# Performance work log

Hardware: AMD Instinct MI355X
Metric: run time of the kernel (lower is better)

The kernel has to match this reference:

```python
import jax, jax.numpy as jnp
import numpy as np

H = 4096        # hidden_size
I = 11008       # intermediate_size
R = 32          # low-rank error-correction rank
NLEV = 16       # int4 -> 16 levels
Q_ZERO = 7.5    # symmetric int4 zero point
Q_STEP = 0.005  # per-channel scale multiplier (keeps dequantized weights ~N(0, 1/sqrt(H)) scale)
LR_SCALE = 0.02 # low-rank correction magnitude


def setup_inputs() -> dict:
    key = jax.random.key(0)
    ks = jax.random.split(key, 13)
    B, S = 2, 2048
    inp = {
        "x": jax.random.normal(ks[0], (B, S, H), jnp.float32),
        "gate_q": jax.random.randint(ks[1], (I, H), 0, NLEV, jnp.int32),
        "gate_scale": jax.random.uniform(ks[2], (I,), jnp.float32),
        "gate_A": jax.random.normal(ks[3], (H, R), jnp.float32),
        "gate_B": jax.random.normal(ks[4], (R, I), jnp.float32),
        "up_q": jax.random.randint(ks[5], (I, H), 0, NLEV, jnp.int32),
        "up_scale": jax.random.uniform(ks[6], (I,), jnp.float32),
        "up_A": jax.random.normal(ks[7], (H, R), jnp.float32),
        "up_B": jax.random.normal(ks[8], (R, I), jnp.float32),
        "down_q": jax.random.randint(ks[9], (H, I), 0, NLEV, jnp.int32),
        "down_scale": jax.random.uniform(ks[10], (H,), jnp.float32),
        "down_A": jax.random.normal(ks[11], (I, R), jnp.float32),
        "down_B": jax.random.normal(ks[12], (R, H), jnp.float32),
    }
    return inp


def _qlinear(x, q, scale, A, Bm):
    # Dequantize int4 weight [out, in] with per-output-channel scale, then
    # y = x @ W^T + LR_SCALE * (x @ A) @ B   (LQER low-rank error correction)
    w = (q.astype(jnp.float32) - Q_ZERO) * (scale * Q_STEP)[:, None]
    y = jnp.einsum('bsh,oh->bso', x, w)
    return y + LR_SCALE * ((x @ A) @ Bm)


def reference(x, gate_q, gate_scale, gate_A, gate_B,
              up_q, up_scale, up_A, up_B,
              down_q, down_scale, down_A, down_B):
    g = _qlinear(x, gate_q, gate_scale, gate_A, gate_B)   # [B,S,I]
    u = _qlinear(x, up_q, up_scale, up_A, up_B)           # [B,S,I]
    h = jax.nn.silu(g) * u                                # SwiGLU gating
    return _qlinear(h, down_q, down_scale, down_A, down_B)  # [B,S,H]
```

## Files before the change

kernel.cpp:

```cpp
#include <hip/hip_runtime.h>
#include <hip/hip_bf16.h>
#include <stdint.h>

#define H_DIM 4096
#define I_DIM 11008
#define M_TOK 4096

typedef __attribute__((ext_vector_type(8))) short short8;
typedef __attribute__((ext_vector_type(4))) float f32x4;
typedef __attribute__((ext_vector_type(4))) int   i32x4;

#define SX_DIV 6.0f
#define QS  (0.0025f * SX_DIV / 127.0f)
#define SH_MAX 768.0f
#define QSD (0.0025f * SH_MAX / 127.0f)

static __device__ __forceinline__ float bf2f(unsigned short u) {
    union { uint32_t i; float f; } v; v.i = ((uint32_t)u) << 16; return v.f;
}
static __device__ __forceinline__ unsigned short f2bf(float f) {
    union { float f; uint32_t i; } v; v.f = f;
    uint32_t r = v.i + 0x7FFF + ((v.i >> 16) & 1);
    return (unsigned short)(r >> 16);
}

static __device__ __forceinline__ void gload16(const void* g, void* l) {
    __builtin_amdgcn_global_load_lds(
        (const __attribute__((address_space(1))) void*)g,
        (__attribute__((address_space(3))) void*)l, 16, 0, 0);
}

__global__ void k_prep_all(
    const float* __restrict__ x,
    const int* __restrict__ gq, const int* __restrict__ uq,
    const int* __restrict__ dq,
    const float* __restrict__ gA, const float* __restrict__ uA,
    const float* __restrict__ dA,
    const float* __restrict__ gB, const float* __restrict__ uB,
    const float* __restrict__ dB,
    unsigned short* __restrict__ xbf, char* __restrict__ xi8,
    char* __restrict__ Wg8, char* __restrict__ Wu8, char* __restrict__ Wd8,
    unsigned short* __restrict__ AgT, unsigned short* __restrict__ AuT,
    unsigned short* __restrict__ AdT,
    unsigned short* __restrict__ BgT, unsigned short* __restrict__ BuT,
    unsigned short* __restrict__ BdT)
{
    const int stride = gridDim.x * blockDim.x;
    const int tid0 = blockIdx.x * blockDim.x + threadIdx.x;
    const int XN4 = (M_TOK * H_DIM) / 4;
    const float SXI = 127.0f / SX_DIV;
    for (int i = tid0; i < XN4; i += stride) {
        f32x4 v = ((const f32x4*)x)[i];
        uint64_t p = (uint64_t)f2bf(v[0]) | ((uint64_t)f2bf(v[1]) << 16) |
                     ((uint64_t)f2bf(v[2]) << 32) | ((uint64_t)f2bf(v[3]) << 48);
        ((uint64_t*)xbf)[i] = p;
        uint32_t q8 = 0;
#pragma unroll
        for (int t = 0; t < 4; t++) {
            int a = (int)lrintf(v[t] * SXI);
            a = a > 127 ? 127 : (a < -127 ? -127 : a);
            q8 |= ((uint32_t)(a & 255)) << (8 * t);
        }
        ((uint32_t*)xi8)[i] = q8;
    }
    const int QN4 = (I_DIM * H_DIM) / 4;
    for (int i = tid0; i < 3 * QN4; i += stride) {
        int j = i; const int* src; char* dst;
        if (j < QN4) { src = gq; dst = Wg8; }
        else if ((j -= QN4) < QN4) { src = uq; dst = Wu8; }
        else { j -= QN4; src = dq; dst = Wd8; }
        i32x4 qv = ((const i32x4*)src)[j];
        uint32_t p = 0;
#pragma unroll
        for (int t = 0; t < 4; t++)
            p |= ((uint32_t)((2 * qv[t] - 15) & 255)) << (8 * t);
        ((uint32_t*)dst)[j] = p;
    }
    const int AT = 32 * H_DIM;
    for (int i = tid0; i < 2 * AT; i += stride) {
        int j = i; const float* src; unsigned short* dst;
        if (j < AT) { src = gA; dst = AgT; } else { j -= AT; src = uA; dst = AuT; }
        int r = j >> 12, k = j & 4095;
        dst[j] = f2bf(src[k * 32 + r]);
    }
    const int ATD = 32 * I_DIM;
    for (int i = tid0; i < ATD; i += stride) {
        int r = i / I_DIM, k = i - r * I_DIM;
        AdT[i] = f2bf(dA[k * 32 + r]);
    }
    const int TBI = I_DIM * 32, TBH = H_DIM * 32;
    for (int i = tid0; i < 2 * TBI + TBH; i += stride) {
        int j = i; const float* src; unsigned short* dst; int N;
        if (j < TBI) { src = gB; dst = BgT; N = I_DIM; }
        else if ((j -= TBI) < TBI) { src = uB; dst = BuT; N = I_DIM; }
        else { j -= TBI; src = dB; dst = BdT; N = H_DIM; }
        int n = j >> 5, r = j & 31;
        dst[j] = f2bf(src[r * N + n]);
    }
}

__global__ __launch_bounds__(512) void k_Tdual(
    const unsigned short* __restrict__ xbf,
    const unsigned short* __restrict__ AgT,
    const unsigned short* __restrict__ AuT,
    unsigned short* __restrict__ Tg,
    unsigned short* __restrict__ Tu)
{
    __shared__ float red[8 * 1024];
    const int wid = threadIdx.x >> 6, lane = threadIdx.x & 63;
    const int base = blockIdx.x * 16;
    const int l15 = lane & 15, kg = (lane >> 4) * 8;
    const int KC = H_DIM / 8;
    const int k0w = wid * KC;
    f32x4 g0 = {}, g1 = {}, u0 = {}, u1 = {};
    for (int k0 = k0w; k0 < k0w + KC; k0 += 32) {
        short8 af  = *(const short8*)&xbf[(size_t)(base + l15) * H_DIM + k0 + kg];
        short8 bg0 = *(const short8*)&AgT[(size_t)l15 * H_DIM + k0 + kg];
        short8 bg1 = *(const short8*)&AgT[(size_t)(16 + l15) * H_DIM + k0 + kg];
        short8 bu0 = *(const short8*)&AuT[(size_t)l15 * H_DIM + k0 + kg];
        short8 bu1 = *(const short8*)&AuT[(size_t)(16 + l15) * H_DIM + k0 + kg];
        g0 = __builtin_amdgcn_mfma_f32_16x16x32_bf16(af, bg0, g0, 0, 0, 0);
        g1 = __builtin_amdgcn_mfma_f32_16x16x32_bf16(af, bg1, g1, 0, 0, 0);
        u0 = __builtin_amdgcn_mfma_f32_16x16x32_bf16(af, bu0, u0, 0, 0, 0);
        u1 = __builtin_amdgcn_mfma_f32_16x16x32_bf16(af, bu1, u1, 0, 0, 0);
    }
    const int q4 = lane >> 4;
    float* rw = red + wid * 1024;
#pragma unroll
    for (int t = 0; t < 4; t++) {
        int row = q4 * 4 + t;
        rw[row * 64 + l15]      = g0[t];
        rw[row * 64 + 16 + l15] = g1[t];
        rw[row * 64 + 32 + l15] = u0[t];
        rw[row * 64 + 48 + l15] = u1[t];
    }
    __syncthreads();
#pragma unroll
    for (int e = threadIdx.x; e < 1024; e += 512) {
        float s = 0.0f;
#pragma unroll
        for (int w = 0; w < 8; w++) s += red[w * 1024 + e];
        int row = e >> 6, c = e & 63;
        int m = base + row;
        if (c < 32) Tg[m * 32 + c] = f2bf(s * 0.02f);
        else        Tu[m * 32 + (c - 32)] = f2bf(s * 0.02f);
    }
}

__global__ __launch_bounds__(512) void k_Tone(
    const unsigned short* __restrict__ in,
    const unsigned short* __restrict__ AT,
    unsigned short* __restrict__ T,
    int K)
{
    __shared__ float red[8 * 512];
    const int wid = threadIdx.x >> 6, lane = threadIdx.x & 63;
    const int base = blockIdx.x * 16;
    const int l15 = lane & 15, kg = (lane >> 4) * 8;
    const int KC = K / 8;
    const int k0w = wid * KC;
    f32x4 a0 = {}, a1 = {};
    for (int k0 = k0w; k0 < k0w + KC; k0 += 32) {
        short8 af = *(const short8*)&in[(size_t)(base + l15) * K + k0 + kg];
        short8 b0 = *(const short8*)&AT[(size_t)l15 * K + k0 + kg];
        short8 b1 = *(const short8*)&AT[(size_t)(16 + l15) * K + k0 + kg];
        a0 = __builtin_amdgcn_mfma_f32_16x16x32_bf16(af, b0, a0, 0, 0, 0);
        a1 = __builtin_amdgcn_mfma_f32_16x16x32_bf16(af, b1, a1, 0, 0, 0);
    }
    const int q4 = lane >> 4;
    float* rw = red + wid * 512;
#pragma unroll
    for (int t = 0; t < 4; t++) {
        int row = q4 * 4 + t;
        rw[row * 32 + l15]      = a0[t];
        rw[row * 32 + 16 + l15] = a1[t];
    }
    __syncthreads();
    if (threadIdx.x < 512) {
        int e = threadIdx.x;
        float s = 0.0f;
#pragma unroll
        for (int w = 0; w < 8; w++) s += red[w * 512 + e];
        int row = e >> 5, c = e & 31;
        T[(base + row) * 32 + c] = f2bf(s * 0.02f);
    }
}

__global__ __launch_bounds__(512, 1) void k_gemmfu8(
    const char* __restrict__ Xq,
    const char* __restrict__ Wg8,
    const char* __restrict__ Wu8,
    const unsigned short* __restrict__ Tg,
    const unsigned short* __restrict__ Tu,
    const unsigned short* __restrict__ BgT,
    const unsigned short* __restrict__ BuT,
    const float* __restrict__ gs, const float* __restrict__ us,
    unsigned short* __restrict__ H,
    char* __restrict__ Hq,
    int M, int NI, int K)
{
    extern __shared__ char dynsmem[];
    char* smem = dynsmem;
    const int tid = threadIdx.x, wid = tid >> 6, lane = tid & 63;
    const int wr = wid >> 2, wc = wid & 3;

    const int gx = NI >> 7;
    const int nwg = gx * (M >> 8);
    int orig = blockIdx.y * gx + blockIdx.x;
    int q8 = nwg >> 3, r8 = nwg & 7;
    int xcd = orig & 7, lid = orig >> 3;
    int wg = (xcd < r8 ? xcd * (q8 + 1) : r8 * (q8 + 1) + (xcd - r8) * q8) + lid;
    const int bcol = (wg % gx) << 7;
    const int brow = (wg / gx) << 8;

    const int srow = wid * 16 + (lane >> 2);
    const int scolB = ((lane & 3) ^ ((lane >> 3) & 3)) * 16;
    const char* aSrc  = Xq  + (size_t)(brow + srow) * K + scolB;
    const char* bgSrc = Wg8 + (size_t)(bcol + srow) * K + scolB;
    const char* buSrc = Wu8 + (size_t)(bcol + srow) * K + scolB;
    const int ldwB = wid * 1024;

    i32x4 acc[8][4];
#pragma unroll
    for (int i = 0; i < 8; ++i)
#pragma unroll
        for (int j = 0; j < 4; ++j) acc[i][j] = (i32x4){0, 0, 0, 0};

    i32x4 A0f[4], A1f[4], BgAf[2], BgBf[2], Buf[2];
    const int l15 = lane & 15, q4b = lane >> 4;
    const int ps = (q4b ^ ((l15 >> 1) & 3)) * 16;
    const char* aRd = smem + (wr * 64 + l15) * 64 + ps;
    const char* bRd = smem + 16384 + (wc * 32 + l15) * 64 + ps;
    const int NT = K >> 6;

#define SA0(BB, k0) gload16(aSrc + (k0), smem + (BB)*32768 + ldwB)
#define SA1(BB, k0) gload16(aSrc + 128*(size_t)K + (k0), smem + (BB)*32768 + 8192 + ldwB)
#define SBG(BB, k0) gload16(bgSrc + (k0), smem + (BB)*32768 + 16384 + ldwB)
#define SBU(BB, k0) gload16(buSrc + (k0), smem + (BB)*32768 + 24576 + ldwB)
#define LDA0(BB) { _Pragma("unroll") for (int i4 = 0; i4 < 4; ++i4) \
    A0f[i4] = *(const i32x4*)(aRd + (BB)*32768 + i4*1024); }
#define LDA1(BB) { _Pragma("unroll") for (int i4 = 0; i4 < 4; ++i4) \
    A1f[i4] = *(const i32x4*)(aRd + (BB)*32768 + 8192 + i4*1024); }
#define LDBG(SET, BB) { _Pragma("unroll") for (int j2 = 0; j2 < 2; ++j2) \
    SET[j2] = *(const i32x4*)(bRd + (BB)*32768 + j2*1024); }
#define LDBU(BB) { _Pragma("unroll") for (int j2 = 0; j2 < 2; ++j2) \
    Buf[j2] = *(const i32x4*)(bRd + (BB)*32768 + 8192 + j2*1024); }
#define MFI(AF, BF, IH, JB) { __builtin_amdgcn_s_setprio(1); \
    _Pragma("unroll") for (int i4 = 0; i4 < 4; ++i4) \
    _Pragma("unroll") for (int j2 = 0; j2 < 2; ++j2) \
        acc[(IH)*4+i4][(JB)*2+j2] = __builtin_amdgcn_mfma_i32_16x16x64_i8( \
            AF[i4], BF[j2], acc[(IH)*4+i4][(JB)*2+j2], 0, 0, 0); \
    __builtin_amdgcn_s_setprio(0); }
#define BARR() __builtin_amdgcn_s_barrier()

#define FTILE(BB, BGC, BGN, k2, S2, CERT, RN) { \
    LDBU(BB); \
    BARR(); \
    MFI(A0f, BGC, 0, 0); \
    LDA1(BB); \
    BARR(); \
    if (S2) { SA0(BB, k2); SBG(BB, k2); } \
    MFI(A0f, Buf, 0, 1); \
    if (CERT == 1) asm volatile("s_waitcnt vmcnt(2)" ::: "memory"); \
    if (CERT == 2) asm volatile("s_waitcnt vmcnt(0)" ::: "memory"); \
    BARR(); \
    if (S2) { SBU(BB, k2); } \
    MFI(A1f, Buf, 1, 1); \
    if (RN) { LDA0(1-(BB)); LDBG(BGN, 1-(BB)); } \
    BARR(); \
    if (S2) { SA1(BB, k2); } \
    MFI(A1f, BGC, 1, 0); \
}

    SA0(0, 0); SBG(0, 0); SBU(0, 0); SA1(0, 0);
    SA0(1, 64); SBG(1, 64); SBU(1, 64); SA1(1, 64);
    asm volatile("s_waitcnt vmcnt(4)" ::: "memory");
    BARR();
    LDA0(0); LDBG(BgAf, 0);

    for (int u = 0; u < (NT - 2) / 2; ++u) {
        const int k2a = (2 * u + 2) << 6, k2b = (2 * u + 3) << 6;
        FTILE(0, BgAf, BgBf, k2a, 1, 1, 1);
        FTILE(1, BgBf, BgAf, k2b, 1, 1, 1);
    }
    FTILE(0, BgAf, BgBf, 0, 0, 2, 1);
    FTILE(1, BgBf, BgAf, 0, 0, 0, 0);

#undef FTILE
#undef BARR
#undef MFI
#undef LDBU
#undef LDBG
#undef LDA1
#undef LDA0
#undef SBU
#undef SBG
#undef SA1
#undef SA0

    __builtin_amdgcn_s_barrier();
    {
        const int scolH = (lane & 3) * 8;
        gload16(Tg + (size_t)(brow + srow) * 32 + scolH,        smem + ldwB);
        gload16(Tg + (size_t)(brow + 128 + srow) * 32 + scolH,  smem + 8192 + ldwB);
        gload16(Tu + (size_t)(brow + srow) * 32 + scolH,        smem + 16384 + ldwB);
        gload16(Tu + (size_t)(brow + 128 + srow) * 32 + scolH,  smem + 24576 + ldwB);
        gload16(BgT + (size_t)(bcol + srow) * 32 + scolH,       smem + 32768 + ldwB);
        gload16(BuT + (size_t)(bcol + srow) * 32 + scolH,       smem + 40960 + ldwB);
    }
    asm volatile("s_waitcnt vmcnt(0)" ::: "memory");
    __builtin_amdgcn_s_barrier();

    const int fr = l15;
    short8 BgF[2], BuF[2];
#pragma unroll
    for (int j2 = 0; j2 < 2; ++j2) {
        BgF[j2] = *(const short8*)(smem + 32768 + (wc * 32 + j2 * 16 + l15) * 64 + q4b * 16);
        BuF[j2] = *(const short8*)(smem + 40960 + (wc * 32 + j2 * 16 + l15) * 64 + q4b * 16);
    }
    float cg[2], cu[2];
#pragma unroll
    for (int j2 = 0; j2 < 2; ++j2) {
        int n = bcol + wc * 32 + j2 * 16 + fr;
        cg[j2] = gs[n] * QS;
        cu[j2] = us[n] * QS;
    }
    const int q4 = lane >> 4;
    const float HSI = 127.0f / SH_MAX;
#pragma unroll
    for (int i = 0; i < 8; ++i) {
        int trow = (i >> 2) * 128 + wr * 64 + (i & 3) * 16 + l15;
        short8 tgf = *(const short8*)(smem + trow * 64 + q4b * 16);
        short8 tuf = *(const short8*)(smem + 16384 + trow * 64 + q4b * 16);
#pragma unroll
        for (int j2 = 0; j2 < 2; ++j2) {
            f32x4 ag, au;
#pragma unroll
            for (int t = 0; t < 4; ++t) {
                ag[t] = (float)acc[i][j2][t] * cg[j2];
                au[t] = (float)acc[i][2 + j2][t] * cu[j2];
            }
            ag = __builtin_amdgcn_mfma_f32_16x16x32_bf16(tgf, BgF[j2], ag, 0, 0, 0);
            au = __builtin_amdgcn_mfma_f32_16x16x32_bf16(tuf, BuF[j2], au, 0, 0, 0);
#pragma unroll
            for (int t = 0; t < 4; ++t) {
                int m = brow + (i >> 2) * 128 + wr * 64 + (i & 3) * 16 + q4 * 4 + t;
                int n = bcol + wc * 32 + j2 * 16 + fr;
                float g = ag[t];
                float s = g / (1.0f + __expf(-g));
                float h = s * au[t];
                H[(size_t)m * NI + n] = f2bf(h);
                int a = (int)lrintf(h * HSI);
                a = a > 127 ? 127 : (a < -127 ? -127 : a);
                Hq[(size_t)m * NI + n] = (char)a;
            }
        }
    }
}

__global__ __launch_bounds__(512, 1) void k_gemmd8(
    const char* __restrict__ Hq,
    const char* __restrict__ Wd8,
    const unsigned short* __restrict__ Td,
    const unsigned short* __restrict__ BdT,
    const float* __restrict__ ds,
    float* __restrict__ C,
    int M, int N, int K)
{
    extern __shared__ char dynsmem[];
    char* smem = dynsmem;
    const int tid = threadIdx.x, wid = tid >> 6, lane = tid & 63;
    const int wr = wid >> 2, wc = wid & 3;

    const int gx = N >> 8;
    const int nwg = gx * (M >> 8);
    int orig = blockIdx.y * gx + blockIdx.x;
    int q8 = nwg >> 3, r8 = nwg & 7;
    int xcd = orig & 7, lid = orig >> 3;
    int wg = (xcd < r8 ? xcd * (q8 + 1) : r8 * (q8 + 1) + (xcd - r8) * q8) + lid;
    const int bcol = (wg % gx) << 8;
    const int brow = (wg / gx) << 8;

    const int srow = wid * 16 + (lane >> 2);
    const int scolB = ((lane & 3) ^ ((lane >> 3) & 3)) * 16;
    const char* aSrc  = Hq  + (size_t)(brow + srow) * K + scolB;
    const char* bgSrc = Wd8 + (size_t)(bcol + srow) * K + scolB;
    const char* buSrc = Wd8 + (size_t)(bcol + 128 + srow) * K + scolB;
    const int ldwB = wid * 1024;

    i32x4 acc[8][4];
#pragma unroll
    for (int i = 0; i < 8; ++i)
#pragma unroll
        for (int j = 0; j < 4; ++j) acc[i][j] = (i32x4){0, 0, 0, 0};

    i32x4 A0f[4], A1f[4], BgAf[2], BgBf[2], Buf[2];
    const int l15 = lane & 15, q4b = lane >> 4;
    const int ps = (q4b ^ ((l15 >> 1) & 3)) * 16;
    const char* aRd = smem + (wr * 64 + l15) * 64 + ps;
    const char* bRd = smem + 16384 + (wc * 32 + l15) * 64 + ps;
    const int NT = K >> 6;

#define SA0(BB, k0) gload16(aSrc + (k0), smem + (BB)*32768 + ldwB)
#define SA1(BB, k0) gload16(aSrc + 128*(size_t)K + (k0), smem + (BB)*32768 + 8192 + ldwB)
#define SBG(BB, k0) gload16(bgSrc + (k0), smem + (BB)*32768 + 16384 + ldwB)
#define SBU(BB, k0) gload16(buSrc + (k0), smem + (BB)*32768 + 24576 + ldwB)
#define LDA0(BB) { _Pragma("unroll") for (int i4 = 0; i4 < 4; ++i4) \
    A0f[i4] = *(const i32x4*)(aRd + (BB)*32768 + i4*1024); }
#define LDA1(BB) { _Pragma("unroll") for (int i4 = 0; i4 < 4; ++i4) \
    A1f[i4] = *(const i32x4*)(aRd + (BB)*32768 + 8192 + i4*1024); }
#define LDBG(SET, BB) { _Pragma("unroll") for (int j2 = 0; j2 < 2; ++j2) \
    SET[j2] = *(const i32x4*)(bRd + (BB)*32768 + j2*1024); }
#define LDBU(BB) { _Pragma("unroll") for (int j2 = 0; j2 < 2; ++j2) \
    Buf[j2] = *(const i32x4*)(bRd + (BB)*32768 + 8192 + j2*1024); }
#define MFI(AF, BF, IH, JB) { __builtin_amdgcn_s_setprio(1); \
    _Pragma("unroll") for (int i4 = 0; i4 < 4; ++i4) \
    _Pragma("unroll") for (int j2 = 0; j2 < 2; ++j2) \
        acc[(IH)*4+i4][(JB)*2+j2] = __builtin_amdgcn_mfma_i32_16x16x64_i8( \
            AF[i4], BF[j2], acc[(IH)*4+i4][(JB)*2+j2], 0, 0, 0); \
    __builtin_amdgcn_s_setprio(0); }
#define BARR() __builtin_amdgcn_s_barrier()

#define FTILE(BB, BGC, BGN, k2, S2, CERT, RN) { \
    LDBU(BB); \
    BARR(); \
    MFI(A0f, BGC, 0, 0); \
    LDA1(BB); \
    BARR(); \
    if (S2) { SA0(BB, k2); SBG(BB, k2); } \
    MFI(A0f, Buf, 0, 1); \
    if (CERT == 1) asm volatile("s_waitcnt vmcnt(2)" ::: "memory"); \
    if (CERT == 2) asm volatile("s_waitcnt vmcnt(0)" ::: "memory"); \
    BARR(); \
    if (S2) { SBU(BB, k2); } \
    MFI(A1f, Buf, 1, 1); \
    if (RN) { LDA0(1-(BB)); LDBG(BGN, 1-(BB)); } \
    BARR(); \
    if (S2) { SA1(BB, k2); } \
    MFI(A1f, BGC, 1, 0); \
}

    SA0(0, 0); SBG(0, 0); SBU(0, 0); SA1(0, 0);
    SA0(1, 64); SBG(1, 64); SBU(1, 64); SA1(1, 64);
    asm volatile("s_waitcnt vmcnt(4)" ::: "memory");
    BARR();
    LDA0(0); LDBG(BgAf, 0);

    for (int u = 0; u < (NT - 2) / 2; ++u) {
        const int k2a = (2 * u + 2) << 6, k2b = (2 * u + 3) << 6;
        FTILE(0, BgAf, BgBf, k2a, 1, 1, 1);
        FTILE(1, BgBf, BgAf, k2b, 1, 1, 1);
    }
    FTILE(0, BgAf, BgBf, 0, 0, 2, 1);
    FTILE(1, BgBf, BgAf, 0, 0, 0, 0);

#undef FTILE
#undef BARR
#undef MFI
#undef LDBU
#undef LDBG
#undef LDA1
#undef LDA0
#undef SBU
#undef SBG
#undef SA1
#undef SA0

    __builtin_amdgcn_s_barrier();
    {
        const int scolH = (lane & 3) * 8;
        gload16(Td + (size_t)(brow + srow) * 32 + scolH,         smem + ldwB);
        gload16(Td + (size_t)(brow + 128 + srow) * 32 + scolH,   smem + 8192 + ldwB);
        gload16(BdT + (size_t)(bcol + srow) * 32 + scolH,        smem + 16384 + ldwB);
        gload16(BdT + (size_t)(bcol + 128 + srow) * 32 + scolH,  smem + 24576 + ldwB);
    }
    asm volatile("s_waitcnt vmcnt(0)" ::: "memory");
    __builtin_amdgcn_s_barrier();

    const int fr = l15;
    short8 Bd0[2], Bd1[2];
#pragma unroll
    for (int j2 = 0; j2 < 2; ++j2) {
        Bd0[j2] = *(const short8*)(smem + 16384 + (wc * 32 + j2 * 16 + l15) * 64 + q4b * 16);
        Bd1[j2] = *(const short8*)(smem + 24576 + (wc * 32 + j2 * 16 + l15) * 64 + q4b * 16);
    }
    float c0[2], c1[2];
#pragma unroll
    for (int j2 = 0; j2 < 2; ++j2) {
        int n0 = bcol + wc * 32 + j2 * 16 + fr;
        c0[j2] = ds[n0] * QSD;
        c1[j2] = ds[n0 + 128] * QSD;
    }
    const int q4 = lane >> 4;
#pragma unroll
    for (int i = 0; i < 8; ++i) {
        int trow = (i >> 2) * 128 + wr * 64 + (i & 3) * 16 + l15;
        short8 tdf = *(const short8*)(smem + trow * 64 + q4b * 16);
#pragma unroll
        for (int j2 = 0; j2 < 2; ++j2) {
            f32x4 a0, a1;
#pragma unroll
            for (int t = 0; t < 4; ++t) {
                a0[t] = (float)acc[i][j2][t] * c0[j2];
                a1[t] = (float)acc[i][2 + j2][t] * c1[j2];
            }
            a0 = __builtin_amdgcn_mfma_f32_16x16x32_bf16(tdf, Bd0[j2], a0, 0, 0, 0);
            a1 = __builtin_amdgcn_mfma_f32_16x16x32_bf16(tdf, Bd1[j2], a1, 0, 0, 0);
#pragma unroll
            for (int t = 0; t < 4; ++t) {
                int m = brow + (i >> 2) * 128 + wr * 64 + (i & 3) * 16 + q4 * 4 + t;
                int n = bcol + wc * 32 + j2 * 16 + fr;
                C[(size_t)m * N + n] = a0[t];
                C[(size_t)m * N + n + 128] = a1[t];
            }
        }
    }
}

extern "C" void kernel_launch(void* const* d_in, const int* in_sizes, int n_in,
                              void* d_out, int out_size, void* d_ws, size_t ws_size,
                              hipStream_t stream) {
    (void)in_sizes; (void)n_in; (void)out_size; (void)ws_size;
    const float* x          = (const float*)d_in[0];
    const int*   gate_q     = (const int*)d_in[1];
    const float* gate_scale = (const float*)d_in[2];
    const float* gate_A     = (const float*)d_in[3];
    const float* gate_B     = (const float*)d_in[4];
    const int*   up_q       = (const int*)d_in[5];
    const float* up_scale   = (const float*)d_in[6];
    const float* up_A       = (const float*)d_in[7];
    const float* up_B       = (const float*)d_in[8];
    const int*   down_q     = (const int*)d_in[9];
    const float* down_scale = (const float*)d_in[10];
    const float* down_A     = (const float*)d_in[11];
    const float* down_B     = (const float*)d_in[12];

    char* ws = (char*)d_ws;
    size_t off = 0;
    auto alloc = [&](size_t bytes) {
        void* p = ws + off; off += (bytes + 255) & ~(size_t)255; return p;
    };
    unsigned short* xbf  = (unsigned short*)alloc((size_t)M_TOK * H_DIM * 2);
    char*           xi8  = (char*)alloc((size_t)M_TOK * H_DIM);
    char*           Wg8  = (char*)alloc((size_t)I_DIM * H_DIM);
    char*           Wu8  = (char*)alloc((size_t)I_DIM * H_DIM);
    char*           Wd8  = (char*)alloc((size_t)H_DIM * I_DIM);
    unsigned short* hbuf = (unsigned short*)alloc((size_t)M_TOK * I_DIM * 2);
    char*           hq   = (char*)alloc((size_t)M_TOK * I_DIM);
    unsigned short* Tg   = (unsigned short*)alloc((size_t)M_TOK * 32 * 2);
    unsigned short* Tu   = (unsigned short*)alloc((size_t)M_TOK * 32 * 2);
    unsigned short* Td   = (unsigned short*)alloc((size_t)M_TOK * 32 * 2);
    unsigned short* AgT  = (unsigned short*)alloc((size_t)32 * H_DIM * 2);
    unsigned short* AuT  = (unsigned short*)alloc((size_t)32 * H_DIM * 2);
    unsigned short* AdT  = (unsigned short*)alloc((size_t)32 * I_DIM * 2);
    unsigned short* BgT  = (unsigned short*)alloc((size_t)I_DIM * 32 * 2);
    unsigned short* BuT  = (unsigned short*)alloc((size_t)I_DIM * 32 * 2);
    unsigned short* BdT  = (unsigned short*)alloc((size_t)H_DIM * 32 * 2);

    (void)hipFuncSetAttribute((const void*)k_gemmfu8,
        hipFuncAttributeMaxDynamicSharedMemorySize, 65536);
    (void)hipFuncSetAttribute((const void*)k_gemmd8,
        hipFuncAttributeMaxDynamicSharedMemorySize, 65536);

    k_prep_all<<<2048, 256, 0, stream>>>(x, gate_q, up_q, down_q,
                                         gate_A, up_A, down_A,
                                         gate_B, up_B, down_B,
                                         xbf, xi8, Wg8, Wu8, Wd8, AgT, AuT, AdT,
                                         BgT, BuT, BdT);

    k_Tdual<<<M_TOK / 16, 512, 0, stream>>>(xbf, AgT, AuT, Tg, Tu);

    k_gemmfu8<<<dim3(I_DIM / 128, M_TOK / 256), 512, 65536, stream>>>(
        xi8, Wg8, Wu8, Tg, Tu, BgT, BuT, gate_scale, up_scale,
        hbuf, hq, M_TOK, I_DIM, H_DIM);

    k_Tone<<<M_TOK / 16, 512, 0, stream>>>(hbuf, AdT, Td, I_DIM);

    k_gemmd8<<<dim3(H_DIM / 256, M_TOK / 256), 512, 65536, stream>>>(
        hq, Wd8, Td, BdT, down_scale, (float*)d_out, M_TOK, H_DIM, I_DIM);
}
```

Before: 776.4 us.

## Switch int8 GEMM kernels from 16x16x64 to 32x32x32 MFMA tiles

Both int8 GEMM kernels (fused gate/up and down) now use 32x32x32 i8 MFMA instructions with 32x32 accumulator tiles instead of 16x16x64. The LDS fragment read addressing is rewritten to match the 32-lane layout, and the epilogues use 32x32x16 bf16 MFMAs for the low-rank correction. The k-loop and setup are shared through macros. The aim is fewer MFMA issues and fewer LDS fragment reads per unit of work. The cost is a different output lane-to-row mapping in the epilogue, which may make global stores less coalesced, and a possible change in register pressure.

```diff
diff --git a/kernel.cpp b/kernel.cpp
--- a/kernel.cpp
+++ b/kernel.cpp
@@ -9,6 +9,8 @@
 typedef __attribute__((ext_vector_type(8))) short short8;
 typedef __attribute__((ext_vector_type(4))) float f32x4;
 typedef __attribute__((ext_vector_type(4))) int   i32x4;
+typedef __attribute__((ext_vector_type(16))) int  i32x16;
+typedef __attribute__((ext_vector_type(16))) float f32x16;
 
 #define SX_DIV 6.0f
 #define QS  (0.0025f * SX_DIV / 127.0f)
@@ -186,70 +188,28 @@
     }
 }
 
-__global__ __launch_bounds__(512, 1) void k_gemmfu8(
-    const char* __restrict__ Xq,
-    const char* __restrict__ Wg8,
-    const char* __restrict__ Wu8,
-    const unsigned short* __restrict__ Tg,
-    const unsigned short* __restrict__ Tu,
-    const unsigned short* __restrict__ BgT,
-    const unsigned short* __restrict__ BuT,
-    const float* __restrict__ gs, const float* __restrict__ us,
-    unsigned short* __restrict__ H,
-    char* __restrict__ Hq,
-    int M, int NI, int K)
-{
-    extern __shared__ char dynsmem[];
-    char* smem = dynsmem;
-    const int tid = threadIdx.x, wid = tid >> 6, lane = tid & 63;
-    const int wr = wid >> 2, wc = wid & 3;
-
-    const int gx = NI >> 7;
-    const int nwg = gx * (M >> 8);
-    int orig = blockIdx.y * gx + blockIdx.x;
-    int q8 = nwg >> 3, r8 = nwg & 7;
-    int xcd = orig & 7, lid = orig >> 3;
-    int wg = (xcd < r8 ? xcd * (q8 + 1) : r8 * (q8 + 1) + (xcd - r8) * q8) + lid;
-    const int bcol = (wg % gx) << 7;
-    const int brow = (wg / gx) << 8;
-
-    const int srow = wid * 16 + (lane >> 2);
-    const int scolB = ((lane & 3) ^ ((lane >> 3) & 3)) * 16;
-    const char* aSrc  = Xq  + (size_t)(brow + srow) * K + scolB;
-    const char* bgSrc = Wg8 + (size_t)(bcol + srow) * K + scolB;
-    const char* buSrc = Wu8 + (size_t)(bcol + srow) * K + scolB;
-    const int ldwB = wid * 1024;
-
-    i32x4 acc[8][4];
-#pragma unroll
-    for (int i = 0; i < 8; ++i)
-#pragma unroll
-        for (int j = 0; j < 4; ++j) acc[i][j] = (i32x4){0, 0, 0, 0};
-
-    i32x4 A0f[4], A1f[4], BgAf[2], BgBf[2], Buf[2];
-    const int l15 = lane & 15, q4b = lane >> 4;
-    const int ps = (q4b ^ ((l15 >> 1) & 3)) * 16;
-    const char* aRd = smem + (wr * 64 + l15) * 64 + ps;
-    const char* bRd = smem + 16384 + (wc * 32 + l15) * 64 + ps;
-    const int NT = K >> 6;
 
 #define SA0(BB, k0) gload16(aSrc + (k0), smem + (BB)*32768 + ldwB)
 #define SA1(BB, k0) gload16(aSrc + 128*(size_t)K + (k0), smem + (BB)*32768 + 8192 + ldwB)
 #define SBG(BB, k0) gload16(bgSrc + (k0), smem + (BB)*32768 + 16384 + ldwB)
 #define SBU(BB, k0) gload16(buSrc + (k0), smem + (BB)*32768 + 24576 + ldwB)
-#define LDA0(BB) { _Pragma("unroll") for (int i4 = 0; i4 < 4; ++i4) \
-    A0f[i4] = *(const i32x4*)(aRd + (BB)*32768 + i4*1024); }
-#define LDA1(BB) { _Pragma("unroll") for (int i4 = 0; i4 < 4; ++i4) \
-    A1f[i4] = *(const i32x4*)(aRd + (BB)*32768 + 8192 + i4*1024); }
-#define LDBG(SET, BB) { _Pragma("unroll") for (int j2 = 0; j2 < 2; ++j2) \
-    SET[j2] = *(const i32x4*)(bRd + (BB)*32768 + j2*1024); }
-#define LDBU(BB) { _Pragma("unroll") for (int j2 = 0; j2 < 2; ++j2) \
-    Buf[j2] = *(const i32x4*)(bRd + (BB)*32768 + 8192 + j2*1024); }
-#define MFI(AF, BF, IH, JB) { __builtin_amdgcn_s_setprio(1); \
-    _Pragma("unroll") for (int i4 = 0; i4 < 4; ++i4) \
-    _Pragma("unroll") for (int j2 = 0; j2 < 2; ++j2) \
-        acc[(IH)*4+i4][(JB)*2+j2] = __builtin_amdgcn_mfma_i32_16x16x64_i8( \
-            AF[i4], BF[j2], acc[(IH)*4+i4][(JB)*2+j2], 0, 0, 0); \
+#define LDA0(BB) { _Pragma("unroll") for (int rb = 0; rb < 2; ++rb) { \
+    A0f[rb*2+0] = *(const i32x4*)(aRd0 + (BB)*32768 + rb*2048); \
+    A0f[rb*2+1] = *(const i32x4*)(aRd1 + (BB)*32768 + rb*2048); } }
+#define LDA1(BB) { _Pragma("unroll") for (int rb = 0; rb < 2; ++rb) { \
+    A1f[rb*2+0] = *(const i32x4*)(aRd0 + (BB)*32768 + 8192 + rb*2048); \
+    A1f[rb*2+1] = *(const i32x4*)(aRd1 + (BB)*32768 + 8192 + rb*2048); } }
+#define LDBG(SET, BB) { \
+    SET[0] = *(const i32x4*)(bRd0 + (BB)*32768); \
+    SET[1] = *(const i32x4*)(bRd1 + (BB)*32768); }
+#define LDBU(BB) { \
+    Buf[0] = *(const i32x4*)(bRd0 + (BB)*32768 + 8192); \
+    Buf[1] = *(const i32x4*)(bRd1 + (BB)*32768 + 8192); }
+#define MFI(AF, BF, HALF, MAT) { __builtin_amdgcn_s_setprio(1); \
+    _Pragma("unroll") for (int rb = 0; rb < 2; ++rb) \
+    _Pragma("unroll") for (int ks = 0; ks < 2; ++ks) \
+        acc32[(HALF)*2+rb][MAT] = __builtin_amdgcn_mfma_i32_32x32x32_i8( \
+            AF[rb*2+ks], BF[ks], acc32[(HALF)*2+rb][MAT], 0, 0, 0); \
     __builtin_amdgcn_s_setprio(0); }
 #define BARR() __builtin_amdgcn_s_barrier()
 
@@ -272,31 +232,67 @@
     MFI(A1f, BGC, 1, 0); \
 }
 
-    SA0(0, 0); SBG(0, 0); SBU(0, 0); SA1(0, 0);
-    SA0(1, 64); SBG(1, 64); SBU(1, 64); SA1(1, 64);
-    asm volatile("s_waitcnt vmcnt(4)" ::: "memory");
-    BARR();
-    LDA0(0); LDBG(BgAf, 0);
-
-    for (int u = 0; u < (NT - 2) / 2; ++u) {
-        const int k2a = (2 * u + 2) << 6, k2b = (2 * u + 3) << 6;
-        FTILE(0, BgAf, BgBf, k2a, 1, 1, 1);
-        FTILE(1, BgBf, BgAf, k2b, 1, 1, 1);
-    }
-    FTILE(0, BgAf, BgBf, 0, 0, 2, 1);
-    FTILE(1, BgBf, BgAf, 0, 0, 0, 0);
-
-#undef FTILE
-#undef BARR
-#undef MFI
-#undef LDBU
-#undef LDBG
-#undef LDA1
-#undef LDA0
-#undef SBU
-#undef SBG
-#undef SA1
-#undef SA0
+#define GEMM8_COMMON_SETUP() \
+    const int tid = threadIdx.x, wid = tid >> 6, lane = tid & 63; \
+    const int wr = wid >> 2, wc = wid & 3; \
+    const int srow = wid * 16 + (lane >> 2); \
+    const int scolB = ((lane & 3) ^ ((lane >> 3) & 3)) * 16; \
+    const int ldwB = wid * 1024; \
+    const int l31 = lane & 31, hi = lane >> 5; \
+    const int ps0 = ((hi ^ ((lane >> 1) & 3))) * 16; \
+    const char* aRd0 = smem + (wr * 64 + l31) * 64 + ps0; \
+    const char* aRd1 = smem + (wr * 64 + l31) * 64 + (ps0 ^ 32); \
+    const char* bRd0 = smem + 16384 + (wc * 32 + l31) * 64 + ps0; \
+    const char* bRd1 = smem + 16384 + (wc * 32 + l31) * 64 + (ps0 ^ 32); \
+    i32x16 acc32[4][2]; \
+    _Pragma("unroll") for (int i = 0; i < 4; ++i) \
+    _Pragma("unroll") for (int j = 0; j < 2; ++j) \
+    _Pragma("unroll") for (int r = 0; r < 16; ++r) acc32[i][j][r] = 0; \
+    i32x4 A0f[4], A1f[4], BgAf[2], BgBf[2], Buf[2];
+
+#define GEMM8_KLOOP(NT_) { \
+    SA0(0, 0); SBG(0, 0); SBU(0, 0); SA1(0, 0); \
+    SA0(1, 64); SBG(1, 64); SBU(1, 64); SA1(1, 64); \
+    asm volatile("s_waitcnt vmcnt(4)" ::: "memory"); \
+    BARR(); \
+    LDA0(0); LDBG(BgAf, 0); \
+    for (int u = 0; u < ((NT_) - 2) / 2; ++u) { \
+        const int k2a = (2 * u + 2) << 6, k2b = (2 * u + 3) << 6; \
+        FTILE(0, BgAf, BgBf, k2a, 1, 1, 1); \
+        FTILE(1, BgBf, BgAf, k2b, 1, 1, 1); \
+    } \
+    FTILE(0, BgAf, BgBf, 0, 0, 2, 1); \
+    FTILE(1, BgBf, BgAf, 0, 0, 0, 0); \
+}
+
+__global__ __launch_bounds__(512, 1) void k_gemmfu8(
+    const char* __restrict__ Xq, const char* __restrict__ Wg8,
+    const char* __restrict__ Wu8,
+    const unsigned short* __restrict__ Tg, const unsigned short* __restrict__ Tu,
+    const unsigned short* __restrict__ BgT, const unsigned short* __restrict__ BuT,
+    const float* __restrict__ gs, const float* __restrict__ us,
+    unsigned short* __restrict__ H, char* __restrict__ Hq,
+    int M, int NI, int K)
+{
+    extern __shared__ char dynsmem[];
+    char* smem = dynsmem;
+    GEMM8_COMMON_SETUP();
+
+    const int gx = NI >> 7;
+    const int nwg = gx * (M >> 8);
+    int orig = blockIdx.y * gx + blockIdx.x;
+    int q8 = nwg >> 3, r8 = nwg & 7;
+    int xcd = orig & 7, lid = orig >> 3;
+    int wg = (xcd < r8 ? xcd * (q8 + 1) : r8 * (q8 + 1) + (xcd - r8) * q8) + lid;
+    const int bcol = (wg % gx) << 7;
+    const int brow = (wg / gx) << 8;
+
+    const char* aSrc  = Xq  + (size_t)(brow + srow) * K + scolB;
+    const char* bgSrc = Wg8 + (size_t)(bcol + srow) * K + scolB;
+    const char* buSrc = Wu8 + (size_t)(bcol + srow) * K + scolB;
+    const int NT = K >> 6;
+
+    GEMM8_KLOOP(NT);
 
     __builtin_amdgcn_s_barrier();
     {
@@ -311,66 +307,56 @@
     asm volatile("s_waitcnt vmcnt(0)" ::: "memory");
     __builtin_amdgcn_s_barrier();
 
-    const int fr = l15;
-    short8 BgF[2], BuF[2];
-#pragma unroll
-    for (int j2 = 0; j2 < 2; ++j2) {
-        BgF[j2] = *(const short8*)(smem + 32768 + (wc * 32 + j2 * 16 + l15) * 64 + q4b * 16);
-        BuF[j2] = *(const short8*)(smem + 40960 + (wc * 32 + j2 * 16 + l15) * 64 + q4b * 16);
-    }
-    float cg[2], cu[2];
-#pragma unroll
-    for (int j2 = 0; j2 < 2; ++j2) {
-        int n = bcol + wc * 32 + j2 * 16 + fr;
-        cg[j2] = gs[n] * QS;
-        cu[j2] = us[n] * QS;
-    }
-    const int q4 = lane >> 4;
+    const int n = bcol + wc * 32 + l31;
+    const float cgl = gs[n] * QS, cul = us[n] * QS;
+    const int nrow = wc * 32 + l31;
+    short8 bg1 = *(const short8*)(smem + 32768 + nrow * 64 + hi * 16);
+    short8 bg2 = *(const short8*)(smem + 32768 + nrow * 64 + hi * 16 + 32);
+    short8 bu1 = *(const short8*)(smem + 40960 + nrow * 64 + hi * 16);
+    short8 bu2 = *(const short8*)(smem + 40960 + nrow * 64 + hi * 16 + 32);
     const float HSI = 127.0f / SH_MAX;
 #pragma unroll
-    for (int i = 0; i < 8; ++i) {
-        int trow = (i >> 2) * 128 + wr * 64 + (i & 3) * 16 + l15;
-        short8 tgf = *(const short8*)(smem + trow * 64 + q4b * 16);
-        short8 tuf = *(const short8*)(smem + 16384 + trow * 64 + q4b * 16);
-#pragma unroll
-        for (int j2 = 0; j2 < 2; ++j2) {
-            f32x4 ag, au;
-#pragma unroll
-            for (int t = 0; t < 4; ++t) {
-                ag[t] = (float)acc[i][j2][t] * cg[j2];
-                au[t] = (float)acc[i][2 + j2][t] * cu[j2];
-            }
-            ag = __builtin_amdgcn_mfma_f32_16x16x32_bf16(tgf, BgF[j2], ag, 0, 0, 0);
-            au = __builtin_amdgcn_mfma_f32_16x16x32_bf16(tuf, BuF[j2], au, 0, 0, 0);
-#pragma unroll
-            for (int t = 0; t < 4; ++t) {
-                int m = brow + (i >> 2) * 128 + wr * 64 + (i & 3) * 16 + q4 * 4 + t;
-                int n = bcol + wc * 32 + j2 * 16 + fr;
-                float g = ag[t];
-                float s = g / (1.0f + __expf(-g));
-                float h = s * au[t];
-                H[(size_t)m * NI + n] = f2bf(h);
-                int a = (int)lrintf(h * HSI);
-                a = a > 127 ? 127 : (a < -127 ? -127 : a);
-                Hq[(size_t)m * NI + n] = (char)a;
-            }
+    for (int rb = 0; rb < 4; ++rb) {
+        const int rbh = rb >> 1, rbl = rb & 1;
+        const int trow = rbh * 128 + wr * 64 + rbl * 32 + l31;
+        short8 tg1 = *(const short8*)(smem + trow * 64 + hi * 16);
+        short8 tg2 = *(const short8*)(smem + trow * 64 + hi * 16 + 32);
+        short8 tu1 = *(const short8*)(smem + 16384 + trow * 64 + hi * 16);
+        short8 tu2 = *(const short8*)(smem + 16384 + trow * 64 + hi * 16 + 32);
+        f32x16 vg, vu;
+#pragma unroll
+        for (int r = 0; r < 16; ++r) {
+            vg[r] = (float)acc32[rbh * 2 + rbl][0][r] * cgl;
+            vu[r] = (float)acc32[rbh * 2 + rbl][1][r] * cul;
         }
+        vg = __builtin_amdgcn_mfma_f32_32x32x16_bf16(tg1, bg1, vg, 0, 0, 0);
+        vg = __builtin_amdgcn_mfma_f32_32x32x16_bf16(tg2, bg2, vg, 0, 0, 0);
+        vu = __builtin_amdgcn_mfma_f32_32x32x16_bf16(tu1, bu1, vu, 0, 0, 0);
+        vu = __builtin_amdgcn_mfma_f32_32x32x16_bf16(tu2, bu2, vu, 0, 0, 0);
+#pragma unroll
+        for (int r = 0; r < 16; ++r) {
+            int m = brow + rbh * 128 + wr * 64 + rbl * 32 +
+                    (r & 3) + 8 * (r >> 2) + 4 * hi;
+            float g = vg[r];
+            float s = g / (1.0f + __expf(-g));
+            float h = s * vu[r];
+            H[(size_t)m * NI + n] = f2bf(h);
+            int a = (int)lrintf(h * HSI);
+            a = a > 127 ? 127 : (a < -127 ? -127 : a);
+            Hq[(size_t)m * NI + n] = (char)a;
+        }
     }
 }
 
 __global__ __launch_bounds__(512, 1) void k_gemmd8(
-    const char* __restrict__ Hq,
-    const char* __restrict__ Wd8,
-    const unsigned short* __restrict__ Td,
-    const unsigned short* __restrict__ BdT,
-    const float* __restrict__ ds,
-    float* __restrict__ C,
+    const char* __restrict__ Hq, const char* __restrict__ Wd8,
+    const unsigned short* __restrict__ Td, const unsigned short* __restrict__ BdT,
+    const float* __restrict__ ds, float* __restrict__ C,
     int M, int N, int K)
 {
     extern __shared__ char dynsmem[];
     char* smem = dynsmem;
-    const int tid = threadIdx.x, wid = tid >> 6, lane = tid & 63;
-    const int wr = wid >> 2, wc = wid & 3;
+    GEMM8_COMMON_SETUP();
 
     const int gx = N >> 8;
     const int nwg = gx * (M >> 8);
@@ -381,90 +367,12 @@
     const int bcol = (wg % gx) << 8;
     const int brow = (wg / gx) << 8;
 
-    const int srow = wid * 16 + (lane >> 2);
-    const int scolB = ((lane & 3) ^ ((lane >> 3) & 3)) * 16;
     const char* aSrc  = Hq  + (size_t)(brow + srow) * K + scolB;
     const char* bgSrc = Wd8 + (size_t)(bcol + srow) * K + scolB;
     const char* buSrc = Wd8 + (size_t)(bcol + 128 + srow) * K + scolB;
-    const int ldwB = wid * 1024;
-
-    i32x4 acc[8][4];
-#pragma unroll
-    for (int i = 0; i < 8; ++i)
-#pragma unroll
-        for (int j = 0; j < 4; ++j) acc[i][j] = (i32x4){0, 0, 0, 0};
-
-    i32x4 A0f[4], A1f[4], BgAf[2], BgBf[2], Buf[2];
-    const int l15 = lane & 15, q4b = lane >> 4;
-    const int ps = (q4b ^ ((l15 >> 1) & 3)) * 16;
-    const char* aRd = smem + (wr * 64 + l15) * 64 + ps;
-    const char* bRd = smem + 16384 + (wc * 32 + l15) * 64 + ps;
     const int NT = K >> 6;
 
-#define SA0(BB, k0) gload16(aSrc + (k0), smem + (BB)*32768 + ldwB)
-#define SA1(BB, k0) gload16(aSrc + 128*(size_t)K + (k0), smem + (BB)*32768 + 8192 + ldwB)
-#define SBG(BB, k0) gload16(bgSrc + (k0), smem + (BB)*32768 + 16384 + ldwB)
-#define SBU(BB, k0) gload16(buSrc + (k0), smem + (BB)*32768 + 24576 + ldwB)
-#define LDA0(BB) { _Pragma("unroll") for (int i4 = 0; i4 < 4; ++i4) \
-    A0f[i4] = *(const i32x4*)(aRd + (BB)*32768 + i4*1024); }
-#define LDA1(BB) { _Pragma("unroll") for (int i4 = 0; i4 < 4; ++i4) \
-    A1f[i4] = *(const i32x4*)(aRd + (BB)*32768 + 8192 + i4*1024); }
-#define LDBG(SET, BB) { _Pragma("unroll") for (int j2 = 0; j2 < 2; ++j2) \
-    SET[j2] = *(const i32x4*)(bRd + (BB)*32768 + j2*1024); }
-#define LDBU(BB) { _Pragma("unroll") for (int j2 = 0; j2 < 2; ++j2) \
-    Buf[j2] = *(const i32x4*)(bRd + (BB)*32768 + 8192 + j2*1024); }
-#define MFI(AF, BF, IH, JB) { __builtin_amdgcn_s_setprio(1); \
-    _Pragma("unroll") for (int i4 = 0; i4 < 4; ++i4) \
-    _Pragma("unroll") for (int j2 = 0; j2 < 2; ++j2) \
-        acc[(IH)*4+i4][(JB)*2+j2] = __builtin_amdgcn_mfma_i32_16x16x64_i8( \
-            AF[i4], BF[j2], acc[(IH)*4+i4][(JB)*2+j2], 0, 0, 0); \
-    __builtin_amdgcn_s_setprio(0); }
-#define BARR() __builtin_amdgcn_s_barrier()
-
-#define FTILE(BB, BGC, BGN, k2, S2, CERT, RN) { \
-    LDBU(BB); \
-    BARR(); \
-    MFI(A0f, BGC, 0, 0); \
-    LDA1(BB); \
-    BARR(); \
-    if (S2) { SA0(BB, k2); SBG(BB, k2); } \
-    MFI(A0f, Buf, 0, 1); \
-    if (CERT == 1) asm volatile("s_waitcnt vmcnt(2)" ::: "memory"); \
-    if (CERT == 2) asm volatile("s_waitcnt vmcnt(0)" ::: "memory"); \
-    BARR(); \
-    if (S2) { SBU(BB, k2); } \
-    MFI(A1f, Buf, 1, 1); \
-    if (RN) { LDA0(1-(BB)); LDBG(BGN, 1-(BB)); } \
-    BARR(); \
-    if (S2) { SA1(BB, k2); } \
-    MFI(A1f, BGC, 1, 0); \
-}
-
-    SA0(0, 0); SBG(0, 0); SBU(0, 0); SA1(0, 0);
-    SA0(1, 64); SBG(1, 64); SBU(1, 64); SA1(1, 64);
-    asm volatile("s_waitcnt vmcnt(4)" ::: "memory");
-    BARR();
-    LDA0(0); LDBG(BgAf, 0);
-
-    for (int u = 0; u < (NT - 2) / 2; ++u) {
-        const int k2a = (2 * u + 2) << 6, k2b = (2 * u + 3) << 6;
-        FTILE(0, BgAf, BgBf, k2a, 1, 1, 1);
-        FTILE(1, BgBf, BgAf, k2b, 1, 1, 1);
-    }
-    FTILE(0, BgAf, BgBf, 0, 0, 2, 1);
-    FTILE(1, BgBf, BgAf, 0, 0, 0, 0);
-
-#undef FTILE
-#undef BARR
-#undef MFI
-#undef LDBU
-#undef LDBG
-#undef LDA1
-#undef LDA0
-#undef SBU
-#undef SBG
-#undef SA1
-#undef SA0
+    GEMM8_KLOOP(NT);
 
     __builtin_amdgcn_s_barrier();
     {
@@ -477,42 +385,35 @@
     asm volatile("s_waitcnt vmcnt(0)" ::: "memory");
     __builtin_amdgcn_s_barrier();
 
-    const int fr = l15;
-    short8 Bd0[2], Bd1[2];
-#pragma unroll
-    for (int j2 = 0; j2 < 2; ++j2) {
-        Bd0[j2] = *(const short8*)(smem + 16384 + (wc * 32 + j2 * 16 + l15) * 64 + q4b * 16);
-        Bd1[j2] = *(const short8*)(smem + 24576 + (wc * 32 + j2 * 16 + l15) * 64 + q4b * 16);
-    }
-    float c0[2], c1[2];
-#pragma unroll
-    for (int j2 = 0; j2 < 2; ++j2) {
-        int n0 = bcol + wc * 32 + j2 * 16 + fr;
-        c0[j2] = ds[n0] * QSD;
-        c1[j2] = ds[n0 + 128] * QSD;
-    }
-    const int q4 = lane >> 4;
-#pragma unroll
-    for (int i = 0; i < 8; ++i) {
-        int trow = (i >> 2) * 128 + wr * 64 + (i & 3) * 16 + l15;
-        short8 tdf = *(const short8*)(smem + trow * 64 + q4b * 16);
-#pragma unroll
-        for (int j2 = 0; j2 < 2; ++j2) {
-            f32x4 a0, a1;
-#pragma unroll
-            for (int t = 0; t < 4; ++t) {
-                a0[t] = (float)acc[i][j2][t] * c0[j2];
-                a1[t] = (float)acc[i][2 + j2][t] * c1[j2];
-            }
-            a0 = __builtin_amdgcn_mfma_f32_16x16x32_bf16(tdf, Bd0[j2], a0, 0, 0, 0);
-            a1 = __builtin_amdgcn_mfma_f32_16x16x32_bf16(tdf, Bd1[j2], a1, 0, 0, 0);
-#pragma unroll
-            for (int t = 0; t < 4; ++t) {
-                int m = brow + (i >> 2) * 128 + wr * 64 + (i & 3) * 16 + q4 * 4 + t;
-                int n = bcol + wc * 32 + j2 * 16 + fr;
-                C[(size_t)m * N + n] = a0[t];
-                C[(size_t)m * N + n + 128] = a1[t];
-            }
+    const int n0 = bcol + wc * 32 + l31;
+    const float c0l = ds[n0] * QSD, c1l = ds[n0 + 128] * QSD;
+    const int nrow = wc * 32 + l31;
+    short8 bd01 = *(const short8*)(smem + 16384 + nrow * 64 + hi * 16);
+    short8 bd02 = *(const short8*)(smem + 16384 + nrow * 64 + hi * 16 + 32);
+    short8 bd11 = *(const short8*)(smem + 24576 + nrow * 64 + hi * 16);
+    short8 bd12 = *(const short8*)(smem + 24576 + nrow * 64 + hi * 16 + 32);
+#pragma unroll
+    for (int rb = 0; rb < 4; ++rb) {
+        const int rbh = rb >> 1, rbl = rb & 1;
+        const int trow = rbh * 128 + wr * 64 + rbl * 32 + l31;
+        short8 td1 = *(const short8*)(smem + trow * 64 + hi * 16);
+        short8 td2 = *(const short8*)(smem + trow * 64 + hi * 16 + 32);
+        f32x16 v0, v1;
+#pragma unroll
+        for (int r = 0; r < 16; ++r) {
+            v0[r] = (float)acc32[rbh * 2 + rbl][0][r] * c0l;
+            v1[r] = (float)acc32[rbh * 2 + rbl][1][r] * c1l;
+        }
+        v0 = __builtin_amdgcn_mfma_f32_32x32x16_bf16(td1, bd01, v0, 0, 0, 0);
+        v0 = __builtin_amdgcn_mfma_f32_32x32x16_bf16(td2, bd02, v0, 0, 0, 0);
+        v1 = __builtin_amdgcn_mfma_f32_32x32x16_bf16(td1, bd11, v1, 0, 0, 0);
+        v1 = __builtin_amdgcn_mfma_f32_32x32x16_bf16(td2, bd12, v1, 0, 0, 0);
+#pragma unroll
+        for (int r = 0; r < 16; ++r) {
+            int m = brow + rbh * 128 + wr * 64 + rbl * 32 +
+                    (r & 3) + 8 * (r >> 2) + 4 * hi;
+            C[(size_t)m * N + n0] = v0[r];
+            C[(size_t)m * N + n0 + 128] = v1[r];
         }
     }
 }
```

New measurement: 826.3 us. 6.4% more time.
